# Kernel optimization log

Measured on AMD Instinct MI355X. Metric: run time of the kernel, lower is better.

The kernel has to match this reference:

```python
import jax, jax.numpy as jnp
import numpy as np

K = 3  # involution kernel size
G = 8  # groups


def setup_inputs() -> dict:
    key = jax.random.key(0)
    ks = jax.random.split(key, 5)
    b, c, h, w = 8, 64, 128, 128
    r = 2
    x = jax.random.normal(ks[0], (b, c, h, w), dtype=jnp.float32)
    w_reduce = jax.random.normal(ks[1], (c // r, c), dtype=jnp.float32) * 0.1
    b_reduce = jax.random.normal(ks[2], (c // r,), dtype=jnp.float32) * 0.1
    w_span = jax.random.normal(ks[3], (K * K * G, c // r), dtype=jnp.float32) * 0.1
    b_span = jax.random.normal(ks[4], (K * K * G,), dtype=jnp.float32) * 0.1
    return {"x": x, "w_reduce": w_reduce, "b_reduce": b_reduce,
            "w_span": w_span, "b_span": b_span}


def reference(x, w_reduce, b_reduce, w_span, b_span):
    b, c, h, w = x.shape
    # kernel generation: two 1x1 convs (ss=1 so AvgPool is identity)
    y = jnp.einsum('oc,bchw->bohw', w_reduce, x) + b_reduce[None, :, None, None]
    kern = jnp.einsum('oc,bchw->bohw', w_span, y) + b_span[None, :, None, None]
    kern = kern.reshape(b, G, K * K, h, w)  # per-pixel dynamic kernel
    # unfold: k=3, padding=1, stride=1 -> patches ordered (c, kh, kw) like nn.Unfold
    xp = jnp.pad(x, ((0, 0), (0, 0), (1, 1), (1, 1)))
    patches = jnp.stack([xp[:, :, i:i + h, j:j + w]
                         for i in range(K) for j in range(K)], axis=2)  # (b,c,9,h,w)
    patches = patches.reshape(b, G, c // G, K * K, h, w)
    # multiply by dynamic kernel (broadcast over c//G) and reduce over k*k
    out = jnp.einsum('bgkhw,bgckhw->bgchw', kern, patches)
    return out.reshape(b, c, h, w)
```

## Files before the change

kernel.cpp:

```cpp
#include <hip/hip_runtime.h>


#define HW 16384
#define WPX 128

__global__ void invol_setup(const float* __restrict__ w_reduce,
                            const float* __restrict__ b_reduce,
                            const float* __restrict__ w_span,
                            const float* __restrict__ b_span,
                            float* __restrict__ ws)
{
    const int tid = blockIdx.x * 256 + threadIdx.x;
    if (tid >= 72 * 64) return;
    const int row = tid >> 6;
    const int c   = tid & 63;
    float s = 0.f;
#pragma unroll
    for (int i = 0; i < 32; ++i)
        s = fmaf(w_span[row * 32 + i], w_reduce[i * 64 + c], s);
    ws[72 + (row / 9) * 576 + c * 9 + (row % 9)] = s;
    if (c == 0) {
        float t = b_span[row];
#pragma unroll
        for (int i = 0; i < 32; ++i)
            t = fmaf(w_span[row * 32 + i], b_reduce[i], t);
        ws[row] = t;
    }
}

__global__ __launch_bounds__(256, 4) void invol_main(
    const float* __restrict__ x,
    const float* __restrict__ ws,
    float* __restrict__ out)
{
    const int bid     = blockIdx.x;
    const int logical = (bid & 7) * 256 + (bid >> 3);
    const int o  = logical & 7;
    const int pb = logical >> 3;

    const int P2  = pb * 256 + threadIdx.x;
    const int b   = P2 >> 13;
    const int hw0 = (P2 & 8191) << 1;
    const int h   = hw0 >> 7;
    const int w0  = hw0 & 127;

    const size_t imgoff = (size_t)b * 64 * HW;
    const float* xb  = x + imgoff + hw0;
    const float* Wg  = ws + 72 + o * 576;
    const float* bbg = ws + o * 9;

    float2 kg[9];
#pragma unroll
    for (int j = 0; j < 9; ++j) { const float t = bbg[j]; kg[j] = make_float2(t, t); }

#pragma unroll
    for (int c0 = 0; c0 < 64; c0 += 8) {
        float2 xv[8];
#pragma unroll
        for (int i = 0; i < 8; ++i)
            xv[i] = *reinterpret_cast<const float2*>(xb + (size_t)(c0 + i) * HW);
#pragma unroll
        for (int i = 0; i < 8; ++i) {
#pragma unroll
            for (int j = 0; j < 9; ++j) {
                const float wv = Wg[(c0 + i) * 9 + j];
                kg[j].x = fmaf(wv, xv[i].x, kg[j].x);
                kg[j].y = fmaf(wv, xv[i].y, kg[j].y);
            }
        }
    }

    int rof[3];
#pragma unroll
    for (int t = 0; t < 3; ++t) {
        const int hh = h + t - 1;
        const int hc = hh < 0 ? 0 : (hh > 127 ? 127 : hh);
        rof[t] = (hc - h) * WPX;
        const float m = ((unsigned)hh < 128u) ? 1.f : 0.f;
#pragma unroll
        for (int d = 0; d < 3; ++d) { kg[t * 3 + d].x *= m; kg[t * 3 + d].y *= m; }
    }
    const int dwl = (w0 == 0)   ? 0 : -1;
    const int dwr = (w0 == 126) ? 1 : 2;
    if (w0 == 0)   { kg[0].x = 0.f; kg[3].x = 0.f; kg[6].x = 0.f; }
    if (w0 == 126) { kg[2].y = 0.f; kg[5].y = 0.f; kg[8].y = 0.f; }

#pragma unroll
    for (int ci = 0; ci < 8; ++ci) {
        const int c = o * 8 + ci;
        const float* xc = xb + (size_t)c * HW;
        float2 vC[3];
        float  vL[3], vR[3];
#pragma unroll
        for (int t = 0; t < 3; ++t) {
            vC[t] = *reinterpret_cast<const float2*>(xc + rof[t]);
            vL[t] = xc[rof[t] + dwl];
            vR[t] = xc[rof[t] + dwr];
        }
        float acc0 = 0.f, acc1 = 0.f;
#pragma unroll
        for (int t = 0; t < 3; ++t) {
            acc0 = fmaf(kg[t * 3 + 0].x, vL[t],   acc0);
            acc0 = fmaf(kg[t * 3 + 1].x, vC[t].x, acc0);
            acc0 = fmaf(kg[t * 3 + 2].x, vC[t].y, acc0);
            acc1 = fmaf(kg[t * 3 + 0].y, vC[t].x, acc1);
            acc1 = fmaf(kg[t * 3 + 1].y, vC[t].y, acc1);
            acc1 = fmaf(kg[t * 3 + 2].y, vR[t],   acc1);
        }
        *reinterpret_cast<float2*>(out + imgoff + (size_t)c * HW + hw0) =
            make_float2(acc0, acc1);
    }
}

__global__ __launch_bounds__(256) void invol_fused_fallback(
    const float* __restrict__ x,
    const float* __restrict__ w_reduce,
    const float* __restrict__ b_reduce,
    const float* __restrict__ w_span,
    const float* __restrict__ b_span,
    float* __restrict__ out)
{
    const int pid = blockIdx.x * 256 + threadIdx.x;
    const int b  = pid >> 14;
    const int hw = pid & 16383;
    const int h  = hw >> 7;
    const int w  = hw & 127;
    const float* xb   = x   + (size_t)b * 64 * HW + hw;
    float*       outb = out + (size_t)b * 64 * HW + hw;
    float y[32];
#pragma unroll
    for (int o = 0; o < 32; ++o) y[o] = b_reduce[o];
#pragma unroll 4
    for (int c = 0; c < 64; ++c) {
        const float xc = xb[(size_t)c * HW];
#pragma unroll
        for (int o = 0; o < 32; ++o)
            y[o] = fmaf(w_reduce[o * 64 + c], xc, y[o]);
    }
    for (int g = 0; g < 8; ++g) {
        float kg[9];
#pragma unroll
        for (int k = 0; k < 9; ++k) {
            float s = b_span[g * 9 + k];
#pragma unroll
            for (int i = 0; i < 32; ++i)
                s = fmaf(w_span[(g * 9 + k) * 32 + i], y[i], s);
            kg[k] = s;
        }
#pragma unroll
        for (int ci = 0; ci < 8; ++ci) {
            const int c = g * 8 + ci;
            const float* xc = xb + (size_t)c * HW;
            float acc = 0.f;
#pragma unroll
            for (int k = 0; k < 9; ++k) {
                const int dh = k / 3 - 1, dw = k % 3 - 1;
                const int hh = h + dh, ww = w + dw;
                float v = ((unsigned)hh < 128u && (unsigned)ww < 128u)
                          ? xc[dh * WPX + dw] : 0.f;
                acc = fmaf(kg[k], v, acc);
            }
            outb[(size_t)c * HW] = acc;
        }
    }
}

extern "C" void kernel_launch(void* const* d_in, const int* in_sizes, int n_in,
                              void* d_out, int out_size, void* d_ws, size_t ws_size,
                              hipStream_t stream) {
    const float* x        = (const float*)d_in[0];
    const float* w_reduce = (const float*)d_in[1];
    const float* b_reduce = (const float*)d_in[2];
    const float* w_span   = (const float*)d_in[3];
    const float* b_span   = (const float*)d_in[4];
    float* out = (float*)d_out;

    const size_t ws_needed = (size_t)(72 + 8 * 64 * 9) * sizeof(float);
    if (ws_size >= ws_needed) {
        float* ws = (float*)d_ws;
        invol_setup<<<18, 256, 0, stream>>>(w_reduce, b_reduce, w_span, b_span, ws);
        const int npairs = 8 * 128 * 128 / 2;
        invol_main<<<npairs / 256 * 8, 256, 0, stream>>>(x, ws, out);
    } else {
        const int npix = 8 * 128 * 128;
        invol_fused_fallback<<<npix / 256, 256, 0, stream>>>(
            x, w_reduce, b_reduce, w_span, b_span, out);
    }
}
```

Measured before the change: 46.07 us.

## Compute four groups per block to cut redundant channel reads

Each block now handles four groups (half of the channels) rather than one, so the 64-channel x reads used to generate the dynamic kernels are shared across four groups. This cuts the block count by a factor of four and the redundant kernel-generation input traffic by the same factor. In exchange each thread holds 36 float2 accumulators plus 32 channel outputs, which raises register pressure under the (256,4) launch bound and may cause spills. The channel loop is also no longer unrolled.

```diff
diff --git a/kernel.cpp b/kernel.cpp
--- a/kernel.cpp
+++ b/kernel.cpp
@@ -18,7 +18,7 @@
 #pragma unroll
     for (int i = 0; i < 32; ++i)
         s = fmaf(w_span[row * 32 + i], w_reduce[i * 64 + c], s);
-    ws[72 + (row / 9) * 576 + c * 9 + (row % 9)] = s;
+    ws[72 + (row / 36) * 2304 + c * 36 + (row % 36)] = s;
     if (c == 0) {
         float t = b_span[row];
 #pragma unroll
@@ -34,9 +34,9 @@
     float* __restrict__ out)
 {
     const int bid     = blockIdx.x;
-    const int logical = (bid & 7) * 256 + (bid >> 3);
-    const int o  = logical & 7;
-    const int pb = logical >> 3;
+    const int logical = (bid & 7) * 64 + (bid >> 3);
+    const int half = logical & 1;
+    const int pb   = logical >> 1;
 
     const int P2  = pb * 256 + threadIdx.x;
     const int b   = P2 >> 13;
@@ -46,14 +46,14 @@
 
     const size_t imgoff = (size_t)b * 64 * HW;
     const float* xb  = x + imgoff + hw0;
-    const float* Wg  = ws + 72 + o * 576;
-    const float* bbg = ws + o * 9;
-
-    float2 kg[9];
-#pragma unroll
-    for (int j = 0; j < 9; ++j) { const float t = bbg[j]; kg[j] = make_float2(t, t); }
-
-#pragma unroll
+    const float* Wh  = ws + 72 + half * 2304;
+    const float* bbh = ws + half * 36;
+
+    float2 kg[36];
+#pragma unroll
+    for (int j = 0; j < 36; ++j) { const float t = bbh[j]; kg[j] = make_float2(t, t); }
+
+#pragma unroll 1
     for (int c0 = 0; c0 < 64; c0 += 8) {
         float2 xv[8];
 #pragma unroll
@@ -62,8 +62,8 @@
 #pragma unroll
         for (int i = 0; i < 8; ++i) {
 #pragma unroll
-            for (int j = 0; j < 9; ++j) {
-                const float wv = Wg[(c0 + i) * 9 + j];
+            for (int j = 0; j < 36; ++j) {
+                const float wv = Wh[(c0 + i) * 36 + j];
                 kg[j].x = fmaf(wv, xv[i].x, kg[j].x);
                 kg[j].y = fmaf(wv, xv[i].y, kg[j].y);
             }
@@ -78,16 +78,31 @@
         rof[t] = (hc - h) * WPX;
         const float m = ((unsigned)hh < 128u) ? 1.f : 0.f;
 #pragma unroll
-        for (int d = 0; d < 3; ++d) { kg[t * 3 + d].x *= m; kg[t * 3 + d].y *= m; }
+        for (int gi = 0; gi < 4; ++gi)
+#pragma unroll
+            for (int d = 0; d < 3; ++d) {
+                kg[gi * 9 + t * 3 + d].x *= m;
+                kg[gi * 9 + t * 3 + d].y *= m;
+            }
     }
     const int dwl = (w0 == 0)   ? 0 : -1;
     const int dwr = (w0 == 126) ? 1 : 2;
-    if (w0 == 0)   { kg[0].x = 0.f; kg[3].x = 0.f; kg[6].x = 0.f; }
-    if (w0 == 126) { kg[2].y = 0.f; kg[5].y = 0.f; kg[8].y = 0.f; }
-
-#pragma unroll
-    for (int ci = 0; ci < 8; ++ci) {
-        const int c = o * 8 + ci;
+    if (w0 == 0) {
+#pragma unroll
+        for (int gi = 0; gi < 4; ++gi) {
+            kg[gi * 9 + 0].x = 0.f; kg[gi * 9 + 3].x = 0.f; kg[gi * 9 + 6].x = 0.f;
+        }
+    }
+    if (w0 == 126) {
+#pragma unroll
+        for (int gi = 0; gi < 4; ++gi) {
+            kg[gi * 9 + 2].y = 0.f; kg[gi * 9 + 5].y = 0.f; kg[gi * 9 + 8].y = 0.f;
+        }
+    }
+
+#pragma unroll
+    for (int ci = 0; ci < 32; ++ci) {
+        const int c = half * 32 + ci;
         const float* xc = xb + (size_t)c * HW;
         float2 vC[3];
         float  vL[3], vR[3];
@@ -97,15 +112,16 @@
             vL[t] = xc[rof[t] + dwl];
             vR[t] = xc[rof[t] + dwr];
         }
+        const int gb = (ci >> 3) * 9;
         float acc0 = 0.f, acc1 = 0.f;
 #pragma unroll
         for (int t = 0; t < 3; ++t) {
-            acc0 = fmaf(kg[t * 3 + 0].x, vL[t],   acc0);
-            acc0 = fmaf(kg[t * 3 + 1].x, vC[t].x, acc0);
-            acc0 = fmaf(kg[t * 3 + 2].x, vC[t].y, acc0);
-            acc1 = fmaf(kg[t * 3 + 0].y, vC[t].x, acc1);
-            acc1 = fmaf(kg[t * 3 + 1].y, vC[t].y, acc1);
-            acc1 = fmaf(kg[t * 3 + 2].y, vR[t],   acc1);
+            acc0 = fmaf(kg[gb + t * 3 + 0].x, vL[t],   acc0);
+            acc0 = fmaf(kg[gb + t * 3 + 1].x, vC[t].x, acc0);
+            acc0 = fmaf(kg[gb + t * 3 + 2].x, vC[t].y, acc0);
+            acc1 = fmaf(kg[gb + t * 3 + 0].y, vC[t].x, acc1);
+            acc1 = fmaf(kg[gb + t * 3 + 1].y, vC[t].y, acc1);
+            acc1 = fmaf(kg[gb + t * 3 + 2].y, vR[t],   acc1);
         }
         *reinterpret_cast<float2*>(out + imgoff + (size_t)c * HW + hw0) =
             make_float2(acc0, acc1);
@@ -175,12 +191,12 @@
     const float* b_span   = (const float*)d_in[4];
     float* out = (float*)d_out;
 
-    const size_t ws_needed = (size_t)(72 + 8 * 64 * 9) * sizeof(float);
+    const size_t ws_needed = (size_t)(72 + 2 * 64 * 36) * sizeof(float);
     if (ws_size >= ws_needed) {
         float* ws = (float*)d_ws;
         invol_setup<<<18, 256, 0, stream>>>(w_reduce, b_reduce, w_span, b_span, ws);
         const int npairs = 8 * 128 * 128 / 2;
-        invol_main<<<npairs / 256 * 8, 256, 0, stream>>>(x, ws, out);
+        invol_main<<<npairs / 256 * 2, 256, 0, stream>>>(x, ws, out);
     } else {
         const int npix = 8 * 128 * 128;
         invol_fused_fallback<<<npix / 256, 256, 0, stream>>>(
```

Measured after the change: 74.63 us. 62.0% more time.
